# Kernel optimization log

Hardware: AMD Instinct MI355X
Metric: run time of the kernel (lower is better)

## Reference

```python
import jax, jax.numpy as jnp
import numpy as np

N_NODES = 65536
N_EDGES = 1048576
IN_DIM = 96
HID = 128
OUT = 2 * HID  # GATv2 out_channels (heads=1, concat)
N_ACT = 20
EDGE_DIM = 3
NEG_SLOPE = 0.2
LN_EPS = 1e-5


def _glorot(key, shape):
    fan_in, fan_out = shape[0], shape[1]
    lim = float(np.sqrt(6.0 / (fan_in + fan_out)))
    return jax.random.uniform(key, shape, jnp.float32, -lim, lim)


def setup_inputs() -> dict:
    key = jax.random.key(0)
    ks = jax.random.split(key, 16)
    inputs = jax.random.normal(ks[0], (N_NODES, IN_DIM), jnp.float32)
    edge_index = jax.random.randint(ks[1], (2, N_EDGES), 0, N_NODES, jnp.int32)
    edge_attr = jax.random.normal(ks[2], (N_EDGES, EDGE_DIM), jnp.float32)
    return {
        "inputs": inputs,
        "edge_index": edge_index,
        "edge_attr": edge_attr,
        # MLP base (n_layers=2, layer_norm=True)
        "W0": _glorot(ks[3], (IN_DIM, HID)), "b0": jnp.zeros((HID,), jnp.float32),
        "g0": jnp.ones((HID,), jnp.float32), "be0": jnp.zeros((HID,), jnp.float32),
        "W1": _glorot(ks[4], (HID, HID)), "b1": jnp.zeros((HID,), jnp.float32),
        "g1": jnp.ones((HID,), jnp.float32), "be1": jnp.zeros((HID,), jnp.float32),
        # GATv2Conv params (heads=1)
        "Wl": _glorot(ks[5], (HID, OUT)), "bl": jnp.zeros((OUT,), jnp.float32),
        "Wr": _glorot(ks[6], (HID, OUT)), "br": jnp.zeros((OUT,), jnp.float32),
        "We": _glorot(ks[7], (EDGE_DIM, OUT)),
        "att": _glorot(ks[8], (OUT, 1))[:, 0],
        "Wres": _glorot(ks[9], (HID, OUT)),
        "gat_bias": jnp.zeros((OUT,), jnp.float32),
        # head: ReLU -> LayerNorm(OUT) -> Linear(OUT, n_actions)
        "g2": jnp.ones((OUT,), jnp.float32), "be2": jnp.zeros((OUT,), jnp.float32),
        "Wq": _glorot(ks[10], (OUT, N_ACT)), "bq": jnp.zeros((N_ACT,), jnp.float32),
    }


def _ln(x, g, b):
    mu = jnp.mean(x, axis=-1, keepdims=True)
    var = jnp.mean(jnp.square(x - mu), axis=-1, keepdims=True)
    return (x - mu) * jax.lax.rsqrt(var + LN_EPS) * g + b


def _gatv2(x, edge_index, edge_attr, Wl, bl, Wr, br, We, att, Wres, gat_bias):
    src, dst = edge_index[0], edge_index[1]
    xl = x @ Wl + bl          # [N, OUT]  (source transform)
    xr = x @ Wr + br          # [N, OUT]  (target transform)
    ef = edge_attr @ We       # [E, OUT]
    m = xl[src] + xr[dst] + ef                      # [E, OUT]
    e = jax.nn.leaky_relu(m, NEG_SLOPE) @ att       # [E]
    # softmax over incoming edges per target node
    e_max = jax.ops.segment_max(e, dst, num_segments=N_NODES)
    ex = jnp.exp(e - e_max[dst])
    denom = jax.ops.segment_sum(ex, dst, num_segments=N_NODES)
    alpha = ex / jnp.where(denom == 0, 1.0, denom)[dst]
    out = jax.ops.segment_sum(alpha[:, None] * xl[src], dst, num_segments=N_NODES)
    return out + x @ Wres + gat_bias


def reference(inputs, edge_index, edge_attr, W0, b0, g0, be0, W1, b1, g1, be1,
              Wl, bl, Wr, br, We, att, Wres, gat_bias, g2, be2, Wq, bq):
    x = _ln(jax.nn.relu(inputs @ W0 + b0), g0, be0)
    x = _ln(jax.nn.relu(x @ W1 + b1), g1, be1)
    h = _gatv2(x, edge_index, edge_attr, Wl, bl, Wr, br, We, att, Wres, gat_bias)
    q = _ln(jax.nn.relu(h), g2, be2) @ Wq + bq
    return q
```

## Files before the change

kernel.cpp:

```cpp
#include <hip/hip_runtime.h>
#include <hip/hip_bf16.h>

#define N_NODES 65536
#define N_EDGES 1048576
#define IN_DIM 96
#define HID 128
#define OUTD 256
#define N_ACT 20

typedef unsigned short u16;
typedef unsigned char u8;
typedef unsigned int u32;
typedef __attribute__((ext_vector_type(8))) short bf16x8;
typedef __attribute__((ext_vector_type(4))) float f32x4;
typedef __attribute__((ext_vector_type(2))) float f32x2;

__device__ __forceinline__ float bf2f(u16 v) { return __uint_as_float(((u32)v) << 16); }
__device__ __forceinline__ u16 f2bf(float f) {
    u32 x = __float_as_uint(f);
    return (u16)((x + 0x7fffu + ((x >> 16) & 1u)) >> 16);
}

__device__ __forceinline__ u8 ftofp8_hw(float f) {
    return (u8)((u32)__builtin_amdgcn_cvt_pk_fp8_f32(f, f, 0, false) & 0xffu);
}

template <int CTRL>
__device__ __forceinline__ float dppadd(float p) {
    return p + __uint_as_float((u32)__builtin_amdgcn_update_dpp(
        0, (int)__float_as_uint(p), CTRL, 0xF, 0xF, true));
}
__device__ __forceinline__ float wave_sum_bcast(float p) {
    p = dppadd<0x111>(p);
    p = dppadd<0x112>(p);
    p = dppadd<0x114>(p);
    p = dppadd<0x118>(p);
    p = dppadd<0x142>(p);
    p = dppadd<0x143>(p);
    return __uint_as_float((u32)__builtin_amdgcn_readlane((int)__float_as_uint(p), 63));
}
__device__ __forceinline__ float red16(float p) {
    p = dppadd<0xB1>(p);
    p = dppadd<0x4E>(p);
    p = dppadd<0x141>(p);
    p = dppadd<0x140>(p);
    return p;
}
__device__ __forceinline__ float red32(float p) {
    p = red16(p);
    p = p + __uint_as_float((u32)__builtin_amdgcn_ds_swizzle(
        (int)__float_as_uint(p), 0x401F));
    return p;
}

__global__ __launch_bounds__(256) void k_prep(
    int* __restrict__ deg,
    const float* __restrict__ Wl, const float* __restrict__ Wr, const float* __restrict__ Wres,
    u16* __restrict__ wt,
    const float* __restrict__ W0, u16* __restrict__ wt0,
    const float* __restrict__ W1, u16* __restrict__ wt1,
    const float* __restrict__ Wq, u16* __restrict__ wqB)
{
    int b = blockIdx.x, t = threadIdx.x;
    if (b < 256) {
        deg[b * 256 + t] = 0;
    } else if (b < 640) {
        int idx = (b - 256) * 256 + t;
        int nn = idx >> 7, k = idx & 127;
        float v;
        if (nn < 256) v = Wl[k * OUTD + nn];
        else if (nn < 512) v = Wr[k * OUTD + (nn - 256)];
        else v = Wres[k * OUTD + (nn - 512)];
        wt[idx] = f2bf(v);
    } else if (b < 688) {
        int idx = (b - 640) * 256 + t;
        int nn = idx / 96, k = idx - nn * 96;
        wt0[idx] = f2bf(W0[k * HID + nn]);
    } else if (b < 752) {
        int idx = (b - 688) * 256 + t;
        int nn = idx >> 7, k = idx & 127;
        wt1[idx] = f2bf(W1[k * HID + nn]);
    } else {
        int idx = (b - 752) * 256 + t;
        int tile = idx >> 12, rem = idx & 4095;
        int kk = rem >> 9, ln = (rem >> 3) & 63, j = idx & 7;
        int k = kk * 32 + (ln >> 4) * 8 + j;
        int q = tile * 16 + (ln & 15);
        wqB[idx] = (q < N_ACT) ? f2bf(Wq[k * N_ACT + q]) : (u16)0;
    }
}

__global__ __launch_bounds__(1024) void k_scan(const int* __restrict__ deg, int* __restrict__ off) {
    __shared__ int part[1024];
    int t = threadIdx.x;
    int base = t * 64;
    const int4* d4 = (const int4*)(deg + base);
    int s = 0;
#pragma unroll
    for (int i = 0; i < 16; i++) { int4 v = d4[i]; s += v.x + v.y + v.z + v.w; }
    part[t] = s;
    __syncthreads();
    for (int o = 1; o < 1024; o <<= 1) {
        int v = (t >= o) ? part[t - o] : 0;
        __syncthreads();
        part[t] += v;
        __syncthreads();
    }
    int run = (t == 0) ? 0 : part[t - 1];
    int4* o4 = (int4*)(off + base);
#pragma unroll
    for (int i = 0; i < 16; i++) {
        int4 v = d4[i];
        int4 w;
        w.x = run;
        w.y = run + v.x;
        w.z = w.y + v.y;
        w.w = w.z + v.z;
        run = w.w + v.w;
        o4[i] = w;
    }
    if (t == 1023) off[N_NODES] = run;
}

__global__ __launch_bounds__(256) void k_scatter(
    const int* __restrict__ ei, const float* __restrict__ ea,
    const int* __restrict__ off, const int* __restrict__ rank,
    int4* __restrict__ erec)
{
    int e = blockIdx.x * 256 + threadIdx.x;
    int src = ei[e];
    int dst = ei[N_EDGES + e];
    float a0 = ea[e * 3 + 0];
    float a1 = ea[e * 3 + 1];
    float a2 = ea[e * 3 + 2];
    int pos = off[dst] + rank[e];
    erec[pos] = make_int4(src, __float_as_int(a0), __float_as_int(a1), __float_as_int(a2));
}

__global__ __launch_bounds__(256, 4) void k_fused(
    const float* __restrict__ in,
    const u16* __restrict__ wt0, const u16* __restrict__ wt1, const u16* __restrict__ wt,
    const float* __restrict__ b0, const float* __restrict__ g0, const float* __restrict__ be0,
    const float* __restrict__ b1, const float* __restrict__ g1, const float* __restrict__ be1,
    const float* __restrict__ bl, const float* __restrict__ br, const float* __restrict__ gbias,
    const int* __restrict__ ei, int* __restrict__ deg, int* __restrict__ rank,
    u8* __restrict__ xl8, u16* __restrict__ xr, u16* __restrict__ hres)
{
    if (blockIdx.x >= 512) {
        int e = (blockIdx.x - 512) * 256 + threadIdx.x;
        rank[e] = atomicAdd(deg + ei[N_EDGES + e], 1);
        return;
    }
    int wid = threadIdx.x >> 6, lane = threadIdx.x & 63;
    int l15 = lane & 15, quad = lane >> 4;
    int m0 = (blockIdx.x * 4 + wid) * 32;

    __shared__ u16 xbuf[4][32][136];

    f32x4 acc[2][8];

#pragma unroll
    for (int mt = 0; mt < 2; mt++)
#pragma unroll
        for (int t = 0; t < 8; t++) acc[mt][t] = {0.f, 0.f, 0.f, 0.f};
#pragma unroll
    for (int kk = 0; kk < 3; kk++) {
        bf16x8 af[2];
#pragma unroll
        for (int mt = 0; mt < 2; mt++) {
            const float* ap = in + (long)(m0 + mt * 16 + l15) * IN_DIM + kk * 32 + quad * 8;
            float4 fa = *(const float4*)(ap);
            float4 fb = *(const float4*)(ap + 4);
            af[mt][0] = (short)f2bf(fa.x); af[mt][1] = (short)f2bf(fa.y);
            af[mt][2] = (short)f2bf(fa.z); af[mt][3] = (short)f2bf(fa.w);
            af[mt][4] = (short)f2bf(fb.x); af[mt][5] = (short)f2bf(fb.y);
            af[mt][6] = (short)f2bf(fb.z); af[mt][7] = (short)f2bf(fb.w);
        }
#pragma unroll
        for (int t = 0; t < 8; t++) {
            bf16x8 bf = *(const bf16x8*)(wt0 + (t * 16 + l15) * IN_DIM + kk * 32 + quad * 8);
            acc[0][t] = __builtin_amdgcn_mfma_f32_16x16x32_bf16(af[0], bf, acc[0][t], 0, 0, 0);
            acc[1][t] = __builtin_amdgcn_mfma_f32_16x16x32_bf16(af[1], bf, acc[1][t], 0, 0, 0);
        }
    }
    {
        float bv[8], gv[8], bev[8];
#pragma unroll
        for (int t = 0; t < 8; t++) {
            int col = t * 16 + l15;
            bv[t] = b0[col]; gv[t] = g0[col]; bev[t] = be0[col];
        }
#pragma unroll
        for (int mt = 0; mt < 2; mt++) {
#pragma unroll
            for (int g = 0; g < 4; g++) {
                float s_ = 0.f, q_ = 0.f;
#pragma unroll
                for (int t = 0; t < 8; t++) {
                    float x = fmaxf(acc[mt][t][g] + bv[t], 0.f);
                    acc[mt][t][g] = x;
                    s_ += x;
                    q_ = fmaf(x, x, q_);
                }
                s_ = red16(s_);
                q_ = red16(q_);
                float mu = s_ * (1.f / HID);
                float var = q_ * (1.f / HID) - mu * mu;
                float rs = rsqrtf(fmaxf(var, 0.f) + 1e-5f);
#pragma unroll
                for (int t = 0; t < 8; t++) {
                    float y = (acc[mt][t][g] - mu) * rs * gv[t] + bev[t];
                    xbuf[wid][mt * 16 + quad * 4 + g][t * 16 + l15] = f2bf(y);
                }
            }
        }
    }

#pragma unroll
    for (int mt = 0; mt < 2; mt++)
#pragma unroll
        for (int t = 0; t < 8; t++) acc[mt][t] = {0.f, 0.f, 0.f, 0.f};
#pragma unroll
    for (int kk = 0; kk < 4; kk++) {
        bf16x8 af0 = *(const bf16x8*)(&xbuf[wid][l15][kk * 32 + quad * 8]);
        bf16x8 af1 = *(const bf16x8*)(&xbuf[wid][16 + l15][kk * 32 + quad * 8]);
#pragma unroll
        for (int t = 0; t < 8; t++) {
            bf16x8 bf = *(const bf16x8*)(wt1 + (t * 16 + l15) * HID + kk * 32 + quad * 8);
            acc[0][t] = __builtin_amdgcn_mfma_f32_16x16x32_bf16(af0, bf, acc[0][t], 0, 0, 0);
            acc[1][t] = __builtin_amdgcn_mfma_f32_16x16x32_bf16(af1, bf, acc[1][t], 0, 0, 0);
        }
    }
    {
        float bv[8], gv[8], bev[8];
#pragma unroll
        for (int t = 0; t < 8; t++) {
            int col = t * 16 + l15;
            bv[t] = b1[col]; gv[t] = g1[col]; bev[t] = be1[col];
        }
#pragma unroll
        for (int mt = 0; mt < 2; mt++) {
#pragma unroll
            for (int g = 0; g < 4; g++) {
                float s_ = 0.f, q_ = 0.f;
#pragma unroll
                for (int t = 0; t < 8; t++) {
                    float x = fmaxf(acc[mt][t][g] + bv[t], 0.f);
                    acc[mt][t][g] = x;
                    s_ += x;
                    q_ = fmaf(x, x, q_);
                }
                s_ = red16(s_);
                q_ = red16(q_);
                float mu = s_ * (1.f / HID);
                float var = q_ * (1.f / HID) - mu * mu;
                float rs = rsqrtf(fmaxf(var, 0.f) + 1e-5f);
#pragma unroll
                for (int t = 0; t < 8; t++) {
                    float y = (acc[mt][t][g] - mu) * rs * gv[t] + bev[t];
                    xbuf[wid][mt * 16 + quad * 4 + g][t * 16 + l15] = f2bf(y);
                }
            }
        }
    }

    for (int nT = 0; nT < 3; nT++) {
        for (int h = 0; h < 2; h++) {
            f32x4 pacc[2][8];
#pragma unroll
            for (int mt = 0; mt < 2; mt++)
#pragma unroll
                for (int t = 0; t < 8; t++) pacc[mt][t] = {0.f, 0.f, 0.f, 0.f};
#pragma unroll
            for (int kk = 0; kk < 4; kk++) {
                bf16x8 af0 = *(const bf16x8*)(&xbuf[wid][l15][kk * 32 + quad * 8]);
                bf16x8 af1 = *(const bf16x8*)(&xbuf[wid][16 + l15][kk * 32 + quad * 8]);
#pragma unroll
                for (int t = 0; t < 8; t++) {
                    bf16x8 bf = *(const bf16x8*)(wt + (long)(nT * 256 + h * 128 + t * 16 + l15) * HID + kk * 32 + quad * 8);
                    pacc[0][t] = __builtin_amdgcn_mfma_f32_16x16x32_bf16(af0, bf, pacc[0][t], 0, 0, 0);
                    pacc[1][t] = __builtin_amdgcn_mfma_f32_16x16x32_bf16(af1, bf, pacc[1][t], 0, 0, 0);
                }
            }
            if (nT == 0) {
#pragma unroll
                for (int t = 0; t < 8; t++) {
                    int col = h * 128 + t * 16 + l15;
                    float bvv = bl[col];
#pragma unroll
                    for (int mt = 0; mt < 2; mt++)
#pragma unroll
                        for (int g = 0; g < 4; g++) {
                            xl8[(long)(m0 + mt * 16 + quad * 4 + g) * OUTD + col] = ftofp8_hw(pacc[mt][t][g] + bvv);
                        }
                }
            } else {
                const float* bias = (nT == 1) ? br : gbias;
                u16* dst = (nT == 1) ? xr : hres;
#pragma unroll
                for (int t = 0; t < 8; t++) {
                    int col = h * 128 + t * 16 + l15;
                    float bvv = bias[col];
#pragma unroll
                    for (int mt = 0; mt < 2; mt++)
#pragma unroll
                        for (int g = 0; g < 4; g++) {
                            dst[(long)(m0 + mt * 16 + quad * 4 + g) * OUTD + col] = f2bf(pacc[mt][t][g] + bvv);
                        }
                }
            }
        }
    }
}

__global__ __launch_bounds__(256, 4) void k_agg_fused(
    const int* __restrict__ off, const int4* __restrict__ erec,
    const u8* __restrict__ xl8, const u16* __restrict__ xr, const u16* __restrict__ hres,
    const float* __restrict__ We, const float* __restrict__ att,
    const float* __restrict__ g2, const float* __restrict__ be2,
    const u16* __restrict__ wqB, const float* __restrict__ bq,
    float* __restrict__ out)
{
    int wid = threadIdx.x >> 6, lane = threadIdx.x & 63;
    int half = lane >> 5, l31 = lane & 31;
    int n = blockIdx.x * 4 + wid;
    int j0 = l31 * 8;
    __shared__ __align__(16) u16 ylds[4][256];

    const float LOG2E = 1.44269504088896f;

    f32x2 w0_[4], w1_[4], w2_[4], at_[4], xr_[4];
    {
        float4 a0 = *(const float4*)(We + j0);
        float4 a1 = *(const float4*)(We + j0 + 4);
        w0_[0] = {a0.x, a0.y}; w0_[1] = {a0.z, a0.w}; w0_[2] = {a1.x, a1.y}; w0_[3] = {a1.z, a1.w};
        float4 b0v = *(const float4*)(We + OUTD + j0);
        float4 b1v = *(const float4*)(We + OUTD + j0 + 4);
        w1_[0] = {b0v.x, b0v.y}; w1_[1] = {b0v.z, b0v.w}; w1_[2] = {b1v.x, b1v.y}; w1_[3] = {b1v.z, b1v.w};
        float4 c0 = *(const float4*)(We + 2 * OUTD + j0);
        float4 c1 = *(const float4*)(We + 2 * OUTD + j0 + 4);
        w2_[0] = {c0.x, c0.y}; w2_[1] = {c0.z, c0.w}; w2_[2] = {c1.x, c1.y}; w2_[3] = {c1.z, c1.w};
        float4 t0 = *(const float4*)(att + j0);
        float4 t1 = *(const float4*)(att + j0 + 4);
        at_[0] = {t0.x * LOG2E, t0.y * LOG2E}; at_[1] = {t0.z * LOG2E, t0.w * LOG2E};
        at_[2] = {t1.x * LOG2E, t1.y * LOG2E}; at_[3] = {t1.z * LOG2E, t1.w * LOG2E};
        ushort4 xa = *(const ushort4*)(xr + (long)n * OUTD + j0);
        ushort4 xb = *(const ushort4*)(xr + (long)n * OUTD + j0 + 4);
        xr_[0] = {bf2f(xa.x), bf2f(xa.y)}; xr_[1] = {bf2f(xa.z), bf2f(xa.w)};
        xr_[2] = {bf2f(xb.x), bf2f(xb.y)}; xr_[3] = {bf2f(xb.z), bf2f(xb.w)};
    }

    int beg = off[n], end = off[n + 1];
    int cnt = end - beg;

    float s = 0.f;
    f32x2 a_[4] = {{0.f, 0.f}, {0.f, 0.f}, {0.f, 0.f}, {0.f, 0.f}};

    auto edge_logit = [&](const int4& R, const uint2& V,
                          f32x2& d0, f32x2& d1, f32x2& d2, f32x2& d3) -> float {
        d0 = __builtin_amdgcn_cvt_pk_f32_fp8((int)V.x, false);
        d1 = __builtin_amdgcn_cvt_pk_f32_fp8((int)V.x, true);
        d2 = __builtin_amdgcn_cvt_pk_f32_fp8((int)V.y, false);
        d3 = __builtin_amdgcn_cvt_pk_f32_fp8((int)V.y, true);
        float ea0 = __int_as_float(R.y), ea1 = __int_as_float(R.z), ea2 = __int_as_float(R.w);
        f32x2 e0v = {ea0, ea0}, e1v = {ea1, ea1}, e2v = {ea2, ea2};
        f32x2 m0 = d0 + xr_[0], m1 = d1 + xr_[1], m2 = d2 + xr_[2], m3 = d3 + xr_[3];
        m0 = __builtin_elementwise_fma(e0v, w0_[0], m0);
        m1 = __builtin_elementwise_fma(e0v, w0_[1], m1);
        m2 = __builtin_elementwise_fma(e0v, w0_[2], m2);
        m3 = __builtin_elementwise_fma(e0v, w0_[3], m3);
        m0 = __builtin_elementwise_fma(e1v, w1_[0], m0);
        m1 = __builtin_elementwise_fma(e1v, w1_[1], m1);
        m2 = __builtin_elementwise_fma(e1v, w1_[2], m2);
        m3 = __builtin_elementwise_fma(e1v, w1_[3], m3);
        m0 = __builtin_elementwise_fma(e2v, w2_[0], m0);
        m1 = __builtin_elementwise_fma(e2v, w2_[1], m1);
        m2 = __builtin_elementwise_fma(e2v, w2_[2], m2);
        m3 = __builtin_elementwise_fma(e2v, w2_[3], m3);
        m0 = __builtin_elementwise_max(m0, 0.2f * m0);
        m1 = __builtin_elementwise_max(m1, 0.2f * m1);
        m2 = __builtin_elementwise_max(m2, 0.2f * m2);
        m3 = __builtin_elementwise_max(m3, 0.2f * m3);
        f32x2 pv = m0 * at_[0];
        pv = __builtin_elementwise_fma(m1, at_[1], pv);
        pv = __builtin_elementwise_fma(m2, at_[2], pv);
        pv = __builtin_elementwise_fma(m3, at_[3], pv);
        return pv[0] + pv[1];
    };

    if (cnt > 0) {
        const u8* xbase = xl8 + j0;
        auto ix = [&](int k) { return beg + min(k + half, cnt - 1); };
        int4 R0 = erec[ix(0)];
        int4 R1 = erec[ix(2)];
        int4 R2 = erec[ix(4)];
        int4 R3 = erec[ix(6)];
        uint2 V0 = *(const uint2*)(xbase + (long)R0.x * OUTD);
        uint2 V1 = *(const uint2*)(xbase + (long)R1.x * OUTD);
#pragma unroll 1
        for (int i = 0; i < cnt; i += 4) {
            int4 R4 = erec[ix(i + 8)];
            int4 R5 = erec[ix(i + 10)];
            uint2 V2 = *(const uint2*)(xbase + (long)R2.x * OUTD);
            uint2 V3 = *(const uint2*)(xbase + (long)R3.x * OUTD);

            f32x2 dA0, dA1, dA2, dA3, dB0, dB1, dB2, dB3;
            float pA = edge_logit(R0, V0, dA0, dA1, dA2, dA3);
            float pB = edge_logit(R1, V1, dB0, dB1, dB2, dB3);

            pA = red32(pA);
            pB = red32(pB);
            if (i + half >= cnt) pA = -1.0e30f;
            if (i + 2 + half >= cnt) pB = -1.0e30f;

            float eA = __builtin_amdgcn_exp2f(pA);
            float eB = __builtin_amdgcn_exp2f(pB);
            s += eA + eB;

            f32x2 eAv = {eA, eA}, eBv = {eB, eB};
            a_[0] = __builtin_elementwise_fma(eAv, dA0, a_[0]);
            a_[1] = __builtin_elementwise_fma(eAv, dA1, a_[1]);
            a_[2] = __builtin_elementwise_fma(eAv, dA2, a_[2]);
            a_[3] = __builtin_elementwise_fma(eAv, dA3, a_[3]);
            a_[0] = __builtin_elementwise_fma(eBv, dB0, a_[0]);
            a_[1] = __builtin_elementwise_fma(eBv, dB1, a_[1]);
            a_[2] = __builtin_elementwise_fma(eBv, dB2, a_[2]);
            a_[3] = __builtin_elementwise_fma(eBv, dB3, a_[3]);

            R0 = R2; R1 = R3; R2 = R4; R3 = R5;
            V0 = V2; V1 = V3;
        }
        s += __shfl_xor(s, 32);
#pragma unroll
        for (int k = 0; k < 4; k++) {
            a_[k][0] += __shfl_xor(a_[k][0], 32);
            a_[k][1] += __shfl_xor(a_[k][1], 32);
        }
    }

    float inv = (cnt > 0) ? 1.f / s : 0.f;

    ushort4 ha = *(const ushort4*)(hres + (long)n * OUTD + j0);
    ushort4 hb = *(const ushort4*)(hres + (long)n * OUTD + j0 + 4);
    float h[8];
    h[0] = fmaxf(fmaf(a_[0][0], inv, bf2f(ha.x)), 0.f);
    h[1] = fmaxf(fmaf(a_[0][1], inv, bf2f(ha.y)), 0.f);
    h[2] = fmaxf(fmaf(a_[1][0], inv, bf2f(ha.z)), 0.f);
    h[3] = fmaxf(fmaf(a_[1][1], inv, bf2f(ha.w)), 0.f);
    h[4] = fmaxf(fmaf(a_[2][0], inv, bf2f(hb.x)), 0.f);
    h[5] = fmaxf(fmaf(a_[2][1], inv, bf2f(hb.y)), 0.f);
    h[6] = fmaxf(fmaf(a_[3][0], inv, bf2f(hb.z)), 0.f);
    h[7] = fmaxf(fmaf(a_[3][1], inv, bf2f(hb.w)), 0.f);

    float sum = ((h[0] + h[1]) + (h[2] + h[3])) + ((h[4] + h[5]) + (h[6] + h[7]));
    float sq = 0.f;
#pragma unroll
    for (int k = 0; k < 8; k++) sq = fmaf(h[k], h[k], sq);
    sum = wave_sum_bcast(sum);
    sq = wave_sum_bcast(sq);
    float mu = sum * (1.f / (2 * OUTD));
    float var = sq * (1.f / (2 * OUTD)) - mu * mu;
    float rs = rsqrtf(fmaxf(var, 0.f) + 1e-5f);

    {
        int jw = j0 + half * 4;
        float4 gv = *(const float4*)(g2 + jw);
        float4 bv = *(const float4*)(be2 + jw);
        int o0 = half * 4;
        ushort4 yy;
        yy.x = f2bf((h[o0 + 0] - mu) * rs * gv.x + bv.x);
        yy.y = f2bf((h[o0 + 1] - mu) * rs * gv.y + bv.y);
        yy.z = f2bf((h[o0 + 2] - mu) * rs * gv.z + bv.z);
        yy.w = f2bf((h[o0 + 3] - mu) * rs * gv.w + bv.w);
        *(ushort4*)(&ylds[wid][jw]) = yy;
    }
    __syncthreads();

    if (wid < 2) {
        int row = lane & 15, qd = lane >> 4;
        const u16* ab = &ylds[row & 3][qd * 8];
        f32x4 cacc = {0.f, 0.f, 0.f, 0.f};
#pragma unroll
        for (int kk = 0; kk < 8; kk++) {
            bf16x8 afrag = *(const bf16x8*)(ab + kk * 32);
            bf16x8 bfrag = *(const bf16x8*)(wqB + ((((wid << 3) + kk) << 6) + lane) * 8);
            cacc = __builtin_amdgcn_mfma_f32_16x16x32_bf16(afrag, bfrag, cacc, 0, 0, 0);
        }
        if (lane < 16) {
            int q = wid * 16 + lane;
            if (q < N_ACT) {
                float bqv = bq[q];
                long nb = (long)blockIdx.x * 4;
#pragma unroll
                for (int g = 0; g < 4; g++)
                    out[(nb + g) * N_ACT + q] = cacc[g] + bqv;
            }
        }
    }
}

extern "C" void kernel_launch(void* const* d_in, const int* in_sizes, int n_in,
                              void* d_out, int out_size, void* d_ws, size_t ws_size,
                              hipStream_t stream) {
    (void)in_sizes; (void)n_in; (void)out_size; (void)ws_size;
    const float* inp  = (const float*)d_in[0];
    const int*   ei   = (const int*)d_in[1];
    const float* ea   = (const float*)d_in[2];
    const float* W0   = (const float*)d_in[3];
    const float* b0   = (const float*)d_in[4];
    const float* g0   = (const float*)d_in[5];
    const float* be0  = (const float*)d_in[6];
    const float* W1   = (const float*)d_in[7];
    const float* b1   = (const float*)d_in[8];
    const float* g1   = (const float*)d_in[9];
    const float* be1  = (const float*)d_in[10];
    const float* Wl   = (const float*)d_in[11];
    const float* bl   = (const float*)d_in[12];
    const float* Wr   = (const float*)d_in[13];
    const float* br   = (const float*)d_in[14];
    const float* We   = (const float*)d_in[15];
    const float* att  = (const float*)d_in[16];
    const float* Wres = (const float*)d_in[17];
    const float* gbias= (const float*)d_in[18];
    const float* g2   = (const float*)d_in[19];
    const float* be2  = (const float*)d_in[20];
    const float* Wq   = (const float*)d_in[21];
    const float* bq   = (const float*)d_in[22];
    float* out = (float*)d_out;

    char* ws = (char*)d_ws;
    size_t o = 0;
    auto alloc = [&](size_t bytes) -> void* {
        void* p = ws + o;
        o += (bytes + 255) & ~(size_t)255;
        return p;
    };
    u8*    xl8    = (u8*)   alloc((size_t)N_NODES * OUTD);
    u16*   xr     = (u16*)  alloc((size_t)N_NODES * OUTD * 2);
    u16*   hres   = (u16*)  alloc((size_t)N_NODES * OUTD * 2);
    int*   deg    = (int*)  alloc((size_t)N_NODES * 4);
    int*   off    = (int*)  alloc((size_t)(N_NODES + 1) * 4);
    int*   rank   = (int*)  alloc((size_t)N_EDGES * 4);
    int4*  erec   = (int4*) alloc((size_t)N_EDGES * 16);
    u16*   wt     = (u16*)  alloc((size_t)768 * HID * 2);
    u16*   wt0    = (u16*)  alloc((size_t)HID * IN_DIM * 2);
    u16*   wt1    = (u16*)  alloc((size_t)HID * HID * 2);
    u16*   wqB    = (u16*)  alloc((size_t)2 * 8 * 64 * 8 * 2);

    k_prep<<<784, 256, 0, stream>>>(deg, Wl, Wr, Wres, wt, W0, wt0, W1, wt1, Wq, wqB);
    k_fused<<<512 + N_EDGES / 256, 256, 0, stream>>>(inp, wt0, wt1, wt,
        b0, g0, be0, b1, g1, be1, bl, br, gbias, ei, deg, rank, xl8, xr, hres);
    k_scan<<<1, 1024, 0, stream>>>(deg, off);
    k_scatter<<<N_EDGES / 256, 256, 0, stream>>>(ei, ea, off, rank, erec);
    k_agg_fused<<<N_NODES / 4, 256, 0, stream>>>(off, erec, xl8, xr, hres, We, att, g2, be2, wqB, bq, out);
}
```

Baseline: 409.9 us.

## Two-pass bucketed scatter of edge records to localize CSR writes

```diff
diff --git a/kernel.cpp b/kernel.cpp
--- a/kernel.cpp
+++ b/kernel.cpp
@@ -7,6 +7,8 @@
 #define HID 128
 #define OUTD 256
 #define N_ACT 20
+#define NBUCK 1024
+#define BCAP 1280
 
 typedef unsigned short u16;
 typedef unsigned char u8;
@@ -54,7 +56,7 @@
 }
 
 __global__ __launch_bounds__(256) void k_prep(
-    int* __restrict__ deg,
+    int* __restrict__ deg, int* __restrict__ bcur,
     const float* __restrict__ Wl, const float* __restrict__ Wr, const float* __restrict__ Wres,
     u16* __restrict__ wt,
     const float* __restrict__ W0, u16* __restrict__ wt0,
@@ -64,6 +66,7 @@
     int b = blockIdx.x, t = threadIdx.x;
     if (b < 256) {
         deg[b * 256 + t] = 0;
+        if (b < 4) bcur[b * 256 + t] = 0;
     } else if (b < 640) {
         int idx = (b - 256) * 256 + t;
         int nn = idx >> 7, k = idx & 127;
@@ -122,9 +125,10 @@
     if (t == 1023) off[N_NODES] = run;
 }
 
-__global__ __launch_bounds__(256) void k_scatter(
+__global__ __launch_bounds__(256) void k_binA(
     const int* __restrict__ ei, const float* __restrict__ ea,
     const int* __restrict__ off, const int* __restrict__ rank,
+    int* __restrict__ bcur, int* __restrict__ bidp, int4* __restrict__ bidr,
     int4* __restrict__ erec)
 {
     int e = blockIdx.x * 256 + threadIdx.x;
@@ -134,7 +138,26 @@
     float a1 = ea[e * 3 + 1];
     float a2 = ea[e * 3 + 2];
     int pos = off[dst] + rank[e];
-    erec[pos] = make_int4(src, __float_as_int(a0), __float_as_int(a1), __float_as_int(a2));
+    int4 rec = make_int4(src, __float_as_int(a0), __float_as_int(a1), __float_as_int(a2));
+    int b = dst >> 6;
+    int p = atomicAdd(bcur + b, 1);
+    if (p < BCAP) {
+        bidp[b * BCAP + p] = pos;
+        bidr[b * BCAP + p] = rec;
+    } else {
+        erec[pos] = rec;
+    }
+}
+
+__global__ __launch_bounds__(256) void k_binB(
+    const int* __restrict__ bcur, const int* __restrict__ bidp, const int4* __restrict__ bidr,
+    int4* __restrict__ erec)
+{
+    int b = blockIdx.x;
+    int cnt = min(bcur[b], BCAP);
+    for (int i = threadIdx.x; i < cnt; i += 256) {
+        erec[bidp[b * BCAP + i]] = bidr[b * BCAP + i];
+    }
 }
 
 __global__ __launch_bounds__(256, 4) void k_fused(
@@ -542,15 +565,19 @@
     int*   off    = (int*)  alloc((size_t)(N_NODES + 1) * 4);
     int*   rank   = (int*)  alloc((size_t)N_EDGES * 4);
     int4*  erec   = (int4*) alloc((size_t)N_EDGES * 16);
+    int*   bcur   = (int*)  alloc((size_t)NBUCK * 4);
+    int*   bidp   = (int*)  alloc((size_t)NBUCK * BCAP * 4);
+    int4*  bidr   = (int4*) alloc((size_t)NBUCK * BCAP * 16);
     u16*   wt     = (u16*)  alloc((size_t)768 * HID * 2);
     u16*   wt0    = (u16*)  alloc((size_t)HID * IN_DIM * 2);
     u16*   wt1    = (u16*)  alloc((size_t)HID * HID * 2);
     u16*   wqB    = (u16*)  alloc((size_t)2 * 8 * 64 * 8 * 2);
 
-    k_prep<<<784, 256, 0, stream>>>(deg, Wl, Wr, Wres, wt, W0, wt0, W1, wt1, Wq, wqB);
+    k_prep<<<784, 256, 0, stream>>>(deg, bcur, Wl, Wr, Wres, wt, W0, wt0, W1, wt1, Wq, wqB);
     k_fused<<<512 + N_EDGES / 256, 256, 0, stream>>>(inp, wt0, wt1, wt,
         b0, g0, be0, b1, g1, be1, bl, br, gbias, ei, deg, rank, xl8, xr, hres);
     k_scan<<<1, 1024, 0, stream>>>(deg, off);
-    k_scatter<<<N_EDGES / 256, 256, 0, stream>>>(ei, ea, off, rank, erec);
+    k_binA<<<N_EDGES / 256, 256, 0, stream>>>(ei, ea, off, rank, bcur, bidp, bidr, erec);
+    k_binB<<<NBUCK, 256, 0, stream>>>(bcur, bidp, bidr, erec);
     k_agg_fused<<<N_NODES / 4, 256, 0, stream>>>(off, erec, xl8, xr, hres, We, att, g2, be2, wqB, bq, out);
 }
```

Measured after the change: 606.4 us. 1.48x slower.
